# Optimization experiments

Hardware: AMD Instinct MI355X
Metric: run time of the kernel (lower is better)

## Reference

```python
import jax, jax.numpy as jnp
import numpy as np

MOMENTUM = 0.05
EPS = 1e-06


def _gated_ema(x, g):
    """y[t] = (1 - g[t]) * y[t-1] + g[t] * x[t], y[-1] = 0.
    x: (B, C, T), g: (B, 1, T) -> (B, C, T)"""
    xT = jnp.moveaxis(x, -1, 0)  # (T, B, C)
    gT = jnp.moveaxis(g, -1, 0)  # (T, B, 1)
    init = jnp.zeros(x.shape[:-1], x.dtype)  # (B, C)

    def step(carry, inp):
        xt, gt = inp
        carry = (1.0 - gt) * carry + gt * xt
        return carry, carry

    _, ys = jax.lax.scan(step, init, (xT, gT))
    return jnp.moveaxis(ys, 0, -1)


def setup_inputs() -> dict:
    key = jax.random.key(0)
    ks = jax.random.split(key, 6)
    B, C, T = 8, 512, 8192
    return {
        "x": jax.random.normal(ks[0], (B, C, T), dtype=jnp.float32),
        "g": jax.random.uniform(ks[1], (B, 1, T), dtype=jnp.float32),
        "Wa_w": jax.random.normal(ks[2], (1, C, 1), dtype=jnp.float32),
        "Wb_w": jax.random.normal(ks[3], (1, C, 1), dtype=jnp.float32),
        "Wo_w": jax.random.normal(ks[4], (C, 1, 1), dtype=jnp.float32),
        "Wo_b": jax.random.normal(ks[5], (C,), dtype=jnp.float32),
    }


def reference(x, g, Wa_w, Wb_w, Wo_w, Wo_b):
    sg = jax.lax.stop_gradient
    C = x.shape[1]
    g = g * MOMENTUM  # time-varying momentum gate
    # Wa: 1x1 conv C->1 with softmax over input channels (convex combination)
    wa = jax.nn.softmax(Wa_w, axis=1)  # (1, C, 1)
    mean = jnp.sum(wa * _gated_ema(sg(x), g), axis=1, keepdims=True)  # (B, 1, T)
    xc = x - mean
    wb = jax.nn.softmax(Wb_w, axis=1)  # (1, C, 1)
    var = jnp.sum(wb * _gated_ema(jnp.square(sg(xc)), g), axis=1, keepdims=True)  # (B, 1, T)
    xn = xc / jnp.sqrt(var + EPS)
    # Wo: grouped 1x1 conv (groups=C) == per-channel scale + bias
    return xn * Wo_w.reshape(1, C, 1) + Wo_b.reshape(1, C, 1)
```

## Files before the change

kernel.cpp:

```cpp
#include <hip/hip_runtime.h>

constexpr int BB = 8, CC = 512, TT = 8192;
constexpr float MOM = 0.05f, EPSV = 1e-6f;

typedef float v4f __attribute__((ext_vector_type(4)));

__device__ __forceinline__ void wave_incl_affine(float& A, float& B) {
  const int lane = threadIdx.x & 63;
  #pragma unroll
  for (int off = 1; off < 64; off <<= 1) {
    float pA = __shfl_up(A, off, 64);
    float pB = __shfl_up(B, off, 64);
    if (lane >= off) { B = fmaf(A, pB, B); A *= pA; }
  }
}

template <int NW>
__device__ __forceinline__ float block_scan_prev(float A, float B,
                                                 float* wAs, float* wBs) {
  const int lane = threadIdx.x & 63, wid = threadIdx.x >> 6;
  wave_incl_affine(A, B);
  __syncthreads();
  if (lane == 63) { wAs[wid] = A; wBs[wid] = B; }
  __syncthreads();
  float cB = 0.f;
  for (int w = 0; w < wid; ++w) cB = fmaf(wAs[w], cB, wBs[w]);
  float leA = __shfl_up(A, 1, 64);
  float leB = __shfl_up(B, 1, 64);
  if (lane == 0) { leA = 1.f; leB = 0.f; }
  return fmaf(leA, cB, leB);
}

__global__ __launch_bounds__(512) void k_reduce(
    const float* __restrict__ x, const float* __restrict__ Wa,
    const float* __restrict__ Wb, float* __restrict__ sa,
    float* __restrict__ sb, float* __restrict__ sb2) {
  __shared__ float lwa[CC], lwb[CC];
  __shared__ float red[3][8][256];
  __shared__ float xw[32];

  const int tid = threadIdx.x;
  const int lane = tid & 63;
  const int wid = tid >> 6;
  const int b = blockIdx.x >> 5;
  const int t0 = (blockIdx.x & 31) * 256;

  {
    float va = Wa[tid], vb = Wb[tid];
    float ma = va, mb = vb;
    #pragma unroll
    for (int off = 32; off > 0; off >>= 1) {
      ma = fmaxf(ma, __shfl_down(ma, off, 64));
      mb = fmaxf(mb, __shfl_down(mb, off, 64));
    }
    if (lane == 0) { xw[wid] = ma; xw[8 + wid] = mb; }
    __syncthreads();
    ma = xw[0]; mb = xw[8];
    #pragma unroll
    for (int w = 1; w < 8; ++w) { ma = fmaxf(ma, xw[w]); mb = fmaxf(mb, xw[8 + w]); }
    const float ea = expf(va - ma), eb = expf(vb - mb);
    float sA = ea, sB = eb;
    #pragma unroll
    for (int off = 32; off > 0; off >>= 1) {
      sA += __shfl_down(sA, off, 64);
      sB += __shfl_down(sB, off, 64);
    }
    if (lane == 0) { xw[16 + wid] = sA; xw[24 + wid] = sB; }
    __syncthreads();
    sA = xw[16]; sB = xw[24];
    #pragma unroll
    for (int w = 1; w < 8; ++w) { sA += xw[16 + w]; sB += xw[24 + w]; }
    lwa[tid] = ea * (1.f / sA);
    lwb[tid] = eb * (1.f / sB);
  }
  __syncthreads();

  const int t4 = lane * 4;
  const int cbase = wid * 64;
  const float* xp = x + ((size_t)(b * CC + cbase)) * TT + t0 + t4;
  float a0=0,a1=0,a2=0,a3=0, b0=0,b1=0,b2=0,b3=0, q0=0,q1=0,q2=0,q3=0;
  #pragma unroll 8
  for (int cc = 0; cc < 64; ++cc) {
    float4 xv = *(const float4*)(xp + (size_t)cc * TT);
    const float wac = lwa[cbase + cc], wbc = lwb[cbase + cc];
    a0 = fmaf(wac, xv.x, a0); a1 = fmaf(wac, xv.y, a1);
    a2 = fmaf(wac, xv.z, a2); a3 = fmaf(wac, xv.w, a3);
    b0 = fmaf(wbc, xv.x, b0); b1 = fmaf(wbc, xv.y, b1);
    b2 = fmaf(wbc, xv.z, b2); b3 = fmaf(wbc, xv.w, b3);
    q0 = fmaf(wbc * xv.x, xv.x, q0); q1 = fmaf(wbc * xv.y, xv.y, q1);
    q2 = fmaf(wbc * xv.z, xv.z, q2); q3 = fmaf(wbc * xv.w, xv.w, q3);
  }
  red[0][wid][t4+0]=a0; red[0][wid][t4+1]=a1; red[0][wid][t4+2]=a2; red[0][wid][t4+3]=a3;
  red[1][wid][t4+0]=b0; red[1][wid][t4+1]=b1; red[1][wid][t4+2]=b2; red[1][wid][t4+3]=b3;
  red[2][wid][t4+0]=q0; red[2][wid][t4+1]=q1; red[2][wid][t4+2]=q2; red[2][wid][t4+3]=q3;
  __syncthreads();

  if (tid < 64) {
    const int o = tid * 4;
    float oa[4] = {0,0,0,0}, ob[4] = {0,0,0,0}, oq[4] = {0,0,0,0};
    #pragma unroll
    for (int w = 0; w < 8; ++w) {
      #pragma unroll
      for (int k = 0; k < 4; ++k) {
        oa[k] += red[0][w][o+k];
        ob[k] += red[1][w][o+k];
        oq[k] += red[2][w][o+k];
      }
    }
    const size_t dst = (size_t)b * TT + t0 + o;
    *(float4*)(sa  + dst) = make_float4(oa[0], oa[1], oa[2], oa[3]);
    *(float4*)(sb  + dst) = make_float4(ob[0], ob[1], ob[2], ob[3]);
    *(float4*)(sb2 + dst) = make_float4(oq[0], oq[1], oq[2], oq[3]);
  }
}

__global__ __launch_bounds__(1024) void k_scan(const float* __restrict__ g,
                                               const float* __restrict__ sa,
                                               const float* __restrict__ sb,
                                               const float* __restrict__ sb2,
                                               float* __restrict__ mean,
                                               float* __restrict__ inv) {
  constexpr int CH = 8;
  __shared__ float wAs[16], wBs[16];
  const int tid = threadIdx.x;
  const size_t base = (size_t)blockIdx.x * TT + (size_t)tid * CH;

  float gv[CH], av[CH], bv[CH], qv[CH];
  *(v4f*)(gv)     = *(const v4f*)(g   + base);
  *(v4f*)(gv + 4) = *(const v4f*)(g   + base + 4);
  *(v4f*)(av)     = *(const v4f*)(sa  + base);
  *(v4f*)(av + 4) = *(const v4f*)(sa  + base + 4);
  *(v4f*)(bv)     = *(const v4f*)(sb  + base);
  *(v4f*)(bv + 4) = *(const v4f*)(sb  + base + 4);
  *(v4f*)(qv)     = *(const v4f*)(sb2 + base);
  *(v4f*)(qv + 4) = *(const v4f*)(sb2 + base + 4);

  float gt[CH], pa[CH];
  float A = 1.f, Bv = 0.f;
  #pragma unroll
  for (int j = 0; j < CH; ++j) {
    const float gg = gv[j] * MOM;
    gt[j] = gg;
    const float p = gg * av[j];
    pa[j] = p;
    const float a = 1.f - gg;
    A *= a;
    Bv = fmaf(a, Bv, p);
  }
  float m = block_scan_prev<16>(A, Bv, wAs, wBs);

  float m4[CH];
  float A2 = 1.f, B2 = 0.f;
  #pragma unroll
  for (int j = 0; j < CH; ++j) {
    const float a = 1.f - gt[j];
    m = fmaf(a, m, pa[j]);
    m4[j] = m;
    const float vi = fmaf(m, m, fmaf(-2.f * m, bv[j], qv[j]));
    const float pv = gt[j] * vi;
    pa[j] = pv;
    A2 *= a;
    B2 = fmaf(a, B2, pv);
  }
  *(v4f*)(mean + base)     = *(v4f*)(m4);
  *(v4f*)(mean + base + 4) = *(v4f*)(m4 + 4);

  float v = block_scan_prev<16>(A2, B2, wAs, wBs);

  float i4[CH];
  #pragma unroll
  for (int j = 0; j < CH; ++j) {
    v = fmaf(1.f - gt[j], v, pa[j]);
    i4[j] = rsqrtf(v + EPSV);
  }
  *(v4f*)(inv + base)     = *(v4f*)(i4);
  *(v4f*)(inv + base + 4) = *(v4f*)(i4 + 4);
}

__global__ __launch_bounds__(512) void k_out(const float* __restrict__ x,
                                             const float* __restrict__ mean,
                                             const float* __restrict__ inv,
                                             const float* __restrict__ wo,
                                             const float* __restrict__ bo,
                                             float* __restrict__ out) {
  const int lane = threadIdx.x & 63;
  const int wid = threadIdx.x >> 6;
  const int tt = blockIdx.x & 31;
  const int ch = (blockIdx.x >> 5) & 1;
  const int b  = blockIdx.x >> 6;
  const int t0 = tt * 256;
  const int t4 = lane * 4;
  const int cbase = ch * 256 + wid * 32;

  const size_t mi = (size_t)b * TT + t0 + t4;
  const v4f m4 = *(const v4f*)(mean + mi);
  const v4f i4 = *(const v4f*)(inv + mi);

  const size_t off0 = ((size_t)(b * CC + cbase)) * TT + t0 + t4;
  const float* xp = x + off0;
  float* op = out + off0;

  #pragma unroll 8
  for (int cc = 0; cc < 32; ++cc) {
    const int c = cbase + cc;
    const v4f xv = *(const v4f*)(xp + (size_t)cc * TT);
    const v4f o = (xv - m4) * i4 * wo[c] + bo[c];
    __builtin_nontemporal_store(o, (v4f*)(op + (size_t)cc * TT));
  }
}

extern "C" void kernel_launch(void* const* d_in, const int* in_sizes, int n_in,
                              void* d_out, int out_size, void* d_ws, size_t ws_size,
                              hipStream_t stream) {
  const float* x  = (const float*)d_in[0];
  const float* g  = (const float*)d_in[1];
  const float* Wa = (const float*)d_in[2];
  const float* Wb = (const float*)d_in[3];
  const float* Wo = (const float*)d_in[4];
  const float* Bo = (const float*)d_in[5];
  float* out = (float*)d_out;

  constexpr int BT = BB * TT;
  float* ws   = (float*)d_ws;
  float* sa   = ws;
  float* sb   = sa + BT;
  float* sb2  = sb + BT;
  float* mean = sb2 + BT;
  float* inv  = mean + BT;

  k_reduce<<<BB * 32, 512, 0, stream>>>(x, Wa, Wb, sa, sb, sb2);
  k_scan<<<BB, 1024, 0, stream>>>(g, sa, sb, sb2, mean, inv);
  k_out<<<BB * 2 * 32, 512, 0, stream>>>(x, mean, inv, Wo, Bo, out);
}
```

Baseline: 83.97 us.

## Fuse scan into output kernel by redundantly recomputing per-batch scan

```diff
diff --git a/kernel.cpp b/kernel.cpp
--- a/kernel.cpp
+++ b/kernel.cpp
@@ -15,7 +15,6 @@
   }
 }
 
-template <int NW>
 __device__ __forceinline__ float block_scan_prev(float A, float B,
                                                  float* wAs, float* wBs) {
   const int lane = threadIdx.x & 63, wid = threadIdx.x >> 6;
@@ -114,87 +113,86 @@
   }
 }
 
-__global__ __launch_bounds__(1024) void k_scan(const float* __restrict__ g,
-                                               const float* __restrict__ sa,
-                                               const float* __restrict__ sb,
-                                               const float* __restrict__ sb2,
-                                               float* __restrict__ mean,
-                                               float* __restrict__ inv) {
-  constexpr int CH = 8;
-  __shared__ float wAs[16], wBs[16];
+__global__ __launch_bounds__(512) void k_scan_out(
+    const float* __restrict__ x, const float* __restrict__ g,
+    const float* __restrict__ sa, const float* __restrict__ sb,
+    const float* __restrict__ sb2, const float* __restrict__ wo,
+    const float* __restrict__ bo, float* __restrict__ out) {
+  __shared__ float wAs[8], wBs[8];
+  __shared__ float mean_s[256], inv_s[256];
+
   const int tid = threadIdx.x;
-  const size_t base = (size_t)blockIdx.x * TT + (size_t)tid * CH;
-
-  float gv[CH], av[CH], bv[CH], qv[CH];
-  *(v4f*)(gv)     = *(const v4f*)(g   + base);
-  *(v4f*)(gv + 4) = *(const v4f*)(g   + base + 4);
-  *(v4f*)(av)     = *(const v4f*)(sa  + base);
-  *(v4f*)(av + 4) = *(const v4f*)(sa  + base + 4);
-  *(v4f*)(bv)     = *(const v4f*)(sb  + base);
-  *(v4f*)(bv + 4) = *(const v4f*)(sb  + base + 4);
-  *(v4f*)(qv)     = *(const v4f*)(sb2 + base);
-  *(v4f*)(qv + 4) = *(const v4f*)(sb2 + base + 4);
-
-  float gt[CH], pa[CH];
-  float A = 1.f, Bv = 0.f;
-  #pragma unroll
-  for (int j = 0; j < CH; ++j) {
-    const float gg = gv[j] * MOM;
-    gt[j] = gg;
-    const float p = gg * av[j];
-    pa[j] = p;
-    const float a = 1.f - gg;
-    A *= a;
-    Bv = fmaf(a, Bv, p);
-  }
-  float m = block_scan_prev<16>(A, Bv, wAs, wBs);
-
-  float m4[CH];
-  float A2 = 1.f, B2 = 0.f;
-  #pragma unroll
-  for (int j = 0; j < CH; ++j) {
-    const float a = 1.f - gt[j];
-    m = fmaf(a, m, pa[j]);
-    m4[j] = m;
-    const float vi = fmaf(m, m, fmaf(-2.f * m, bv[j], qv[j]));
-    const float pv = gt[j] * vi;
-    pa[j] = pv;
-    A2 *= a;
-    B2 = fmaf(a, B2, pv);
-  }
-  *(v4f*)(mean + base)     = *(v4f*)(m4);
-  *(v4f*)(mean + base + 4) = *(v4f*)(m4 + 4);
-
-  float v = block_scan_prev<16>(A2, B2, wAs, wBs);
-
-  float i4[CH];
-  #pragma unroll
-  for (int j = 0; j < CH; ++j) {
-    v = fmaf(1.f - gt[j], v, pa[j]);
-    i4[j] = rsqrtf(v + EPSV);
-  }
-  *(v4f*)(inv + base)     = *(v4f*)(i4);
-  *(v4f*)(inv + base + 4) = *(v4f*)(i4 + 4);
-}
-
-__global__ __launch_bounds__(512) void k_out(const float* __restrict__ x,
-                                             const float* __restrict__ mean,
-                                             const float* __restrict__ inv,
-                                             const float* __restrict__ wo,
-                                             const float* __restrict__ bo,
-                                             float* __restrict__ out) {
-  const int lane = threadIdx.x & 63;
-  const int wid = threadIdx.x >> 6;
+  const int lane = tid & 63;
+  const int wid = tid >> 6;
   const int tt = blockIdx.x & 31;
   const int ch = (blockIdx.x >> 5) & 1;
   const int b  = blockIdx.x >> 6;
   const int t0 = tt * 256;
+
+  constexpr int CH = 16;
+  const size_t sbase = (size_t)b * TT + (size_t)tid * CH;
+  float gt[CH], pa[CH], mv[CH];
+
+  float A = 1.f, Bv = 0.f;
+  #pragma unroll
+  for (int j = 0; j < CH; j += 4) {
+    const v4f gq = *(const v4f*)(g  + sbase + j);
+    const v4f aq = *(const v4f*)(sa + sbase + j);
+    #pragma unroll
+    for (int k = 0; k < 4; ++k) {
+      const float gg = gq[k] * MOM;
+      gt[j + k] = gg;
+      const float p = gg * aq[k];
+      pa[j + k] = p;
+      const float a = 1.f - gg;
+      A *= a;
+      Bv = fmaf(a, Bv, p);
+    }
+  }
+  float m = block_scan_prev(A, Bv, wAs, wBs);
+
+  float A2 = 1.f, B2 = 0.f;
+  #pragma unroll
+  for (int j = 0; j < CH; j += 4) {
+    const v4f bq = *(const v4f*)(sb  + sbase + j);
+    const v4f qq = *(const v4f*)(sb2 + sbase + j);
+    #pragma unroll
+    for (int k = 0; k < 4; ++k) {
+      const float a = 1.f - gt[j + k];
+      m = fmaf(a, m, pa[j + k]);
+      mv[j + k] = m;
+      const float vi = fmaf(m, m, fmaf(-2.f * m, bq[k], qq[k]));
+      const float pv = gt[j + k] * vi;
+      pa[j + k] = pv;
+      A2 *= a;
+      B2 = fmaf(a, B2, pv);
+    }
+  }
+  float v = block_scan_prev(A2, B2, wAs, wBs);
+
+  const int town = tid - tt * 16;
+  if (town >= 0 && town < 16) {
+    const int o = town * CH;
+    #pragma unroll
+    for (int j = 0; j < CH; ++j) mean_s[o + j] = mv[j];
+  }
+  float iv[CH];
+  #pragma unroll
+  for (int j = 0; j < CH; ++j) {
+    v = fmaf(1.f - gt[j], v, pa[j]);
+    iv[j] = rsqrtf(v + EPSV);
+  }
+  if (town >= 0 && town < 16) {
+    const int o = town * CH;
+    #pragma unroll
+    for (int j = 0; j < CH; ++j) inv_s[o + j] = iv[j];
+  }
+  __syncthreads();
+
   const int t4 = lane * 4;
   const int cbase = ch * 256 + wid * 32;
-
-  const size_t mi = (size_t)b * TT + t0 + t4;
-  const v4f m4 = *(const v4f*)(mean + mi);
-  const v4f i4 = *(const v4f*)(inv + mi);
+  const v4f m4 = *(const v4f*)&mean_s[t4];
+  const v4f i4 = *(const v4f*)&inv_s[t4];
 
   const size_t off0 = ((size_t)(b * CC + cbase)) * TT + t0 + t4;
   const float* xp = x + off0;
@@ -221,14 +219,11 @@
   float* out = (float*)d_out;
 
   constexpr int BT = BB * TT;
-  float* ws   = (float*)d_ws;
-  float* sa   = ws;
-  float* sb   = sa + BT;
-  float* sb2  = sb + BT;
-  float* mean = sb2 + BT;
-  float* inv  = mean + BT;
+  float* ws  = (float*)d_ws;
+  float* sa  = ws;
+  float* sb  = sa + BT;
+  float* sb2 = sb + BT;
 
   k_reduce<<<BB * 32, 512, 0, stream>>>(x, Wa, Wb, sa, sb, sb2);
-  k_scan<<<BB, 1024, 0, stream>>>(g, sa, sb, sb2, mean, inv);
-  k_out<<<BB * 2 * 32, 512, 0, stream>>>(x, mean, inv, Wo, Bo, out);
-}
+  k_scan_out<<<BB * 2 * 32, 512, 0, stream>>>(x, g, sa, sb, sb2, Wo, Bo, out);
+}
```

Result: no change. 84.67 us (+0.8%).
